# Performance work log

Hardware: AMD Instinct MI355X
Metric: run time of the kernel (lower is better)

## Reference

```python
import math
import jax, jax.numpy as jnp
import numpy as np

HEADS = 8
DIM_HEAD = 64
NUM_MEM_KV = 16


def alibi_slopes(heads):
    def pow2_slopes(n):
        start = 2 ** (-(2 ** -(math.log2(n) - 3)))
        return [start * (start ** i) for i in range(n)]
    if math.log2(heads).is_integer():
        return np.asarray(pow2_slopes(heads), dtype=np.float32)
    cp2 = 2 ** math.floor(math.log2(heads))
    extra = pow2_slopes(2 * cp2)[0::2][: heads - cp2]
    return np.asarray(pow2_slopes(cp2) + extra, dtype=np.float32)


def setup_inputs() -> dict:
    key = jax.random.key(0)
    ks = jax.random.split(key, 12)
    b, n, dim = 2, 2048, 512
    h, dh, mem = HEADS, DIM_HEAD, NUM_MEM_KV
    s = 0.02  # weight init scale for numerical sanity
    return {
        "x": jax.random.normal(ks[0], (b, n, dim), jnp.float32),
        "Wq": jax.random.normal(ks[1], (dim, h * dh), jnp.float32) * s,
        "Wk": jax.random.normal(ks[2], (dim, h * dh), jnp.float32) * s,
        "Wv": jax.random.normal(ks[3], (dim, h * dh), jnp.float32) * s,
        "mem_k": jax.random.normal(ks[4], (h, mem, dh), jnp.float32),
        "mem_v": jax.random.normal(ks[5], (h, mem, dh), jnp.float32),
        "pre_proj": jax.random.normal(ks[6], (h, h), jnp.float32),
        "post_proj": jax.random.normal(ks[7], (h, h), jnp.float32),
        "head_scale_params": jnp.ones((1, h, 1, 1), jnp.float32),
        "Wout": jax.random.normal(ks[8], (h * dh, dim), jnp.float32) * s,
        "bout": jnp.zeros((dim,), jnp.float32),
    }


def reference(x, Wq, Wk, Wv, mem_k, mem_v, pre_proj, post_proj,
              head_scale_params, Wout, bout):
    b, n, dim = x.shape
    h, dh, mem = HEADS, DIM_HEAD, NUM_MEM_KV
    scale = dh ** -0.5

    def split_heads(t):  # [b,n,h*dh] -> [b,h,n,dh]
        return t.reshape(b, n, h, dh).transpose(0, 2, 1, 3)

    q = split_heads(x @ Wq)
    k = split_heads(x @ Wk)
    v = split_heads(x @ Wv)

    # prepend learned memory key/values: k,v -> [b,h,mem+n,dh]
    k = jnp.concatenate([jnp.broadcast_to(mem_k, (b, h, mem, dh)), k], axis=2)
    v = jnp.concatenate([jnp.broadcast_to(mem_v, (b, h, mem, dh)), v], axis=2)
    j = mem + n

    dots = jnp.einsum('bhid,bhjd->bhij', q, k) * scale
    # talking heads (pre-softmax)
    dots = jnp.einsum('bhij,hk->bkij', dots, pre_proj)
    # alibi relative positional bias: arange(j) * slope per head
    slopes = jnp.asarray(alibi_slopes(h))  # [h]
    dots = dots + jnp.arange(j, dtype=dots.dtype)[None, None, None, :] * slopes[None, :, None, None]
    # causal mask (mem columns always visible); mask where col-mem > row
    neg = -jnp.finfo(dots.dtype).max
    causal = (jnp.arange(j)[None, :] - mem) > jnp.arange(n)[:, None]  # [n,j]
    dots = jnp.where(causal[None, None], neg, dots)

    attn = jax.nn.softmax(dots, axis=-1)
    # talking heads (post-softmax)
    attn = jnp.einsum('bhij,hk->bkij', attn, post_proj)

    out = jnp.einsum('bhij,bhjd->bhid', attn, v)
    out = out * head_scale_params
    out = out.transpose(0, 2, 1, 3).reshape(b, n, h * dh)
    return out @ Wout + bout
```

## Files before the change

kernel.cpp:

```cpp
#include <hip/hip_runtime.h>
#include <math.h>

namespace {
constexpr int B = 2;
constexpr int N = 2048;
constexpr int DIM = 512;
constexpr int H = 8;
constexpr int MEM = 16;
constexpr int J = MEM + N;
constexpr int CHUNK = 512;
constexpr int CMAXS = 5;
constexpr float S2 = 0.125f * 1.4426950408889634f;
constexpr size_t EPB = 17170432;
}

typedef __attribute__((ext_vector_type(8))) short short8;
typedef __attribute__((ext_vector_type(2))) float floatx2;
typedef __attribute__((ext_vector_type(4))) float floatx4;
typedef __attribute__((ext_vector_type(4))) unsigned short ushortx4;
typedef __attribute__((ext_vector_type(8))) unsigned short ushortx8;
typedef __attribute__((ext_vector_type(4))) unsigned int uintx4;

__device__ inline unsigned short f2bf(float f) {
    unsigned int u = __float_as_uint(f);
    u += 0x7fffu + ((u >> 16) & 1u);
    return (unsigned short)(u >> 16);
}
__device__ inline unsigned int pk2bf(float a, float b) {
    return ((__float_as_uint(a) + 0x8000u) >> 16) |
           ((__float_as_uint(b) + 0x8000u) & 0xffff0000u);
}

__global__ __launch_bounds__(256)
void x_conv(const float* __restrict__ x, unsigned short* __restrict__ x16)
{
    const size_t base = ((size_t)blockIdx.x * 256 + threadIdx.x) * 8;
    const float4 a = *(const float4*)(x + base);
    const float4 b = *(const float4*)(x + base + 4);
    ushortx8 o = { f2bf(a.x), f2bf(a.y), f2bf(a.z), f2bf(a.w),
                   f2bf(b.x), f2bf(b.y), f2bf(b.z), f2bf(b.w) };
    *(ushortx8*)(x16 + base) = o;
}

__global__ __launch_bounds__(256)
void wt_conv(const float* __restrict__ Wq, const float* __restrict__ Wk,
             const float* __restrict__ Wv, const float* __restrict__ Wo,
             unsigned short* __restrict__ tq, unsigned short* __restrict__ tk,
             unsigned short* __restrict__ tv, unsigned short* __restrict__ to_)
{
    const int z = blockIdx.z;
    const float* __restrict__ W = (z == 0) ? Wq : (z == 1) ? Wk : (z == 2) ? Wv : Wo;
    unsigned short* __restrict__ WT = (z == 0) ? tq : (z == 1) ? tk : (z == 2) ? tv : to_;
    const int k0 = blockIdx.x * 64, n0 = blockIdx.y * 64;

    __shared__ __align__(16) unsigned short tile[64][72];
    const int t = threadIdx.x;
    const int rrow = t >> 4, rcol = (t & 15) * 4;
#pragma unroll
    for (int rr = 0; rr < 4; ++rr) {
        const int row = rrow + rr * 16;
        const float4 v = *(const float4*)(W + (size_t)(k0 + row) * DIM + n0 + rcol);
        tile[rcol + 0][row] = f2bf(v.x);
        tile[rcol + 1][row] = f2bf(v.y);
        tile[rcol + 2][row] = f2bf(v.z);
        tile[rcol + 3][row] = f2bf(v.w);
    }
    __syncthreads();
    const int orow = t >> 2, oseg = (t & 3) * 16;
    *(ushortx8*)(WT + (size_t)(n0 + orow) * DIM + k0 + oseg) =
        *(const ushortx8*)(&tile[orow][oseg]);
    *(ushortx8*)(WT + (size_t)(n0 + orow) * DIM + k0 + oseg + 8) =
        *(const ushortx8*)(&tile[orow][oseg + 8]);
}

__global__ __launch_bounds__(256)
void qkv_gemm(const unsigned short* __restrict__ x16, const unsigned short* __restrict__ tq,
              const unsigned short* __restrict__ tk, const unsigned short* __restrict__ tv,
              unsigned short* __restrict__ q16, unsigned short* __restrict__ kcat,
              unsigned short* __restrict__ vt16)
{
    const int which = blockIdx.z;
    const unsigned short* __restrict__ WT = (which == 0) ? tq : (which == 1) ? tk : tv;
    const int t = threadIdx.x;
    const int lane = t & 63, w = t >> 6;
    const int iL = lane & 15, quad = lane >> 4;
    const int mb = blockIdx.x * 64;
    const int n0 = blockIdx.y * 64;

    __shared__ __align__(16) unsigned short As[2][64][32];
    __shared__ __align__(16) unsigned short Bs[2][64][32];

    const int r0 = t >> 2, s8 = (t & 3) * 8;

    floatx4 acc[4];
#pragma unroll
    for (int ng = 0; ng < 4; ++ng) acc[ng] = (floatx4){0.f, 0.f, 0.f, 0.f};

    {
        *(ushortx8*)(&As[0][r0][s8]) =
            *(const ushortx8*)(x16 + (size_t)(mb + r0) * DIM + s8);
        *(ushortx8*)(&Bs[0][r0][s8]) =
            *(const ushortx8*)(WT + (size_t)(n0 + r0) * DIM + s8);
    }
    __syncthreads();

#pragma unroll
    for (int it = 0; it < 16; ++it) {
        const int buf = it & 1;
        if (it + 1 < 16) {
            const int k0 = (it + 1) * 32;
            const ushortx8 av = *(const ushortx8*)(x16 + (size_t)(mb + r0) * DIM + k0 + s8);
            const ushortx8 bv = *(const ushortx8*)(WT + (size_t)(n0 + r0) * DIM + k0 + s8);
            *(ushortx8*)(&As[buf ^ 1][r0][s8]) = av;
            *(ushortx8*)(&Bs[buf ^ 1][r0][s8]) = bv;
        }
        const short8 af = *(const short8*)(&As[buf][w * 16 + iL][quad * 8]);
#pragma unroll
        for (int ng = 0; ng < 4; ++ng) {
            const short8 bf = *(const short8*)(&Bs[buf][ng * 16 + iL][quad * 8]);
            acc[ng] = __builtin_amdgcn_mfma_f32_16x16x32_bf16(af, bf, acc[ng], 0, 0, 0);
        }
        __syncthreads();
    }

    const int mbw = mb + w * 16;
    const int h0 = n0 >> 6;
    if (which == 2) {
#pragma unroll
        for (int ng = 0; ng < 4; ++ng) {
            const int d = ng * 16 + iL;
#pragma unroll
            for (int r = 0; r < 4; ++r) {
                const int m = mbw + quad * 4 + r;
                const int bb = m >> 11, ii = m & (N - 1);
                vt16[((size_t)(bb * H + h0) * 64 + d) * J + MEM + ii] = f2bf(acc[ng][r]);
            }
        }
    } else if (which == 1) {
#pragma unroll
        for (int ng = 0; ng < 4; ++ng) {
            const int d = ng * 16 + iL;
#pragma unroll
            for (int r = 0; r < 4; ++r) {
                const int m = mbw + quad * 4 + r;
                const int bb = m >> 11, ii = m & (N - 1);
                kcat[((size_t)bb * J + MEM + ii) * 512 + h0 * 64 + d] = f2bf(acc[ng][r]);
            }
        }
    } else {
#pragma unroll
        for (int ng = 0; ng < 4; ++ng) {
            const int d = ng * 16 + iL;
#pragma unroll
            for (int r = 0; r < 4; ++r) {
                const int m = mbw + quad * 4 + r;
                const int bb = m >> 11, ii = m & (N - 1);
                q16[((size_t)(bb * H + h0) * N + ii) * 64 + d] = f2bf(acc[ng][r]);
            }
        }
    }
}

__global__ void memkv_copy(const float* __restrict__ mem_k, const float* __restrict__ mem_v,
                           unsigned short* __restrict__ kcat, unsigned short* __restrict__ vt16)
{
    const int idx = blockIdx.x * 256 + threadIdx.x;
    if (idx >= H * MEM * 64) return;
    const int h0 = idx >> 10;
    const int rd = idx & 1023;
    const int r = rd >> 6, d = rd & 63;
    const unsigned short kk = f2bf(mem_k[idx]);
    const unsigned short vv = f2bf(mem_v[idx]);
#pragma unroll
    for (int bb = 0; bb < B; ++bb) {
        kcat[((size_t)bb * J + r) * 512 + h0 * 64 + d] = kk;
        vt16[((size_t)(bb * H + h0) * 64 + d) * J + r] = vv;
    }
}

__global__ __launch_bounds__(512, 4)
void attn_scores(const unsigned short* __restrict__ qb, const unsigned short* __restrict__ kc,
                 const float* __restrict__ prep, float* __restrict__ lbuf,
                 unsigned short* __restrict__ e16)
{
    const int tt = blockIdx.x, c = 4 - blockIdx.y, b = blockIdx.z;
    const int i0 = tt * 16;
    const int jlim = i0 + 32;
    const int jstart = c * CHUNK;
    if (jstart >= jlim) return;
    const int jend = min(jstart + CHUNK, jlim);
    const int nwin = (jend - jstart) >> 4;

    __shared__ __align__(16) unsigned short k_s[2][16][520];

    const int t = threadIdx.x;
    const int lane = t & 63, w = t >> 6;
    const int iL = lane & 15, quad = lane >> 4;
    const int i = i0 + iL;

    const size_t krowbase = (size_t)b * J * 512;

    auto STAGE = [&](int buf, int jw0) {
#pragma unroll
        for (int rr = 0; rr < 2; ++rr) {
            const int row = rr * 8 + w;
            const int j = jw0 + row;
            const char* src = (const char*)(kc + krowbase + (size_t)j * 512);
            __builtin_amdgcn_global_load_lds(
                (const __attribute__((address_space(1))) unsigned int*)(src + lane * 16),
                (__attribute__((address_space(3))) unsigned int*)(&k_s[buf][row][0]),
                16, 0, 0);
        }
    };

    STAGE(0, jstart);

    float pr[8];
#pragma unroll
    for (int h0 = 0; h0 < 8; ++h0) pr[h0] = prep[h0 * 8 + w];
    short8 qf[16];
#pragma unroll
    for (int ks = 0; ks < 16; ++ks) {
        const ushortx8 raw = *(const ushortx8*)(
            qb + ((size_t)(b * H + (ks >> 1)) * N + i0 + iL) * 64 + (ks & 1) * 32 + quad * 8);
        const float s = pr[ks >> 1];
        uintx4 u;
#pragma unroll
        for (int e2 = 0; e2 < 4; ++e2) {
            const float f0 = __uint_as_float((unsigned int)raw[e2 * 2] << 16) * s;
            const float f1 = __uint_as_float((unsigned int)raw[e2 * 2 + 1] << 16) * s;
            u[e2] = pk2bf(f0, f1);
        }
        qf[ks] = __builtin_bit_cast(short8, u);
    }
    __syncthreads();

    const float sl = 1.4426950408889634f / (float)(2 << w);
    const size_t ebase = (size_t)b * EPB + (size_t)(8 * tt * tt + 24 * tt) * 128;
    float l_acc = 0.f;

    for (int n = 0; n < nwin; ++n) {
        const int buf = n & 1;
        if (n + 1 < nwin) STAGE(buf ^ 1, jstart + (n + 1) * 16);
        const int jw0 = jstart + n * 16;

        floatx4 aE = {0.f, 0.f, 0.f, 0.f}, aO = {0.f, 0.f, 0.f, 0.f};
#pragma unroll
        for (int ks = 0; ks < 16; ks += 2) {
            const short8 f0 = *(const short8*)(&k_s[buf][iL][ks * 32 + quad * 8]);
            const short8 f1 = *(const short8*)(&k_s[buf][iL][(ks + 1) * 32 + quad * 8]);
            aE = __builtin_amdgcn_mfma_f32_16x16x32_bf16(f0, qf[ks], aE, 0, 0, 0);
            aO = __builtin_amdgcn_mfma_f32_16x16x32_bf16(f1, qf[ks + 1], aO, 0, 0, 0);
        }
        const floatx4 a = aE + aO;

#pragma unroll
        for (int r = 0; r < 4; ++r) {
            const int j = jw0 + quad * 4 + r;
            const int jm = j - MEM;
            const float e = (jm <= i)
                ? exp2f(fmaf(a[r], S2, sl * (float)(jm - i))) : 0.f;
            l_acc += e;
            e16[ebase + ((size_t)j * 16 + iL) * 8 + w] = f2bf(e);
        }
        __syncthreads();
    }

    l_acc += __shfl_xor(l_acc, 16);
    l_acc += __shfl_xor(l_acc, 32);
    if (quad == 0)
        atomicAdd(lbuf + ((size_t)(b * 128 + tt) * 8 + w) * 16 + iL, l_acc);
}

__global__ __launch_bounds__(256)
void attn_pv2(const unsigned short* __restrict__ e16, const unsigned short* __restrict__ vt,
              const float* __restrict__ postp, const float* __restrict__ hsp,
              const float* __restrict__ lbuf, float* __restrict__ ao)
{
    const int tt = blockIdx.x, c = 4 - blockIdx.y, b = blockIdx.z;
    const int i0 = tt * 16;
    const int jlim = i0 + 32;
    const int jstart = c * CHUNK;
    if (jstart >= jlim) return;
    const int jend = min(jstart + CHUNK, jlim);
    const int nw = (jend - jstart + 31) >> 5;

    __shared__ __align__(16) unsigned short p2s[2][8][16][40];
    __shared__ __align__(16) float post_s[64];

    const int t = threadIdx.x;
    if (t < 64) post_s[t] = postp[t] * hsp[t & 7];

    const int lane = t & 63, w = t >> 6;
    const int iL = lane & 15, quad = lane >> 4;
    const int dW = w * 16 + iL;
    const int i_p = t & 15;
    const int jj = t >> 4;
    const size_t ebase = (size_t)b * EPB + (size_t)(8 * tt * tt + 24 * tt) * 128;
    const unsigned short* __restrict__ ep = e16 + ebase + (size_t)i_p * 8;

    float linv[8];
#pragma unroll
    for (int h1 = 0; h1 < 8; ++h1)
        linv[h1] = 1.0f / lbuf[((size_t)(b * 128 + tt) * 8 + h1) * 16 + i_p];

    floatx4 y[8];
#pragma unroll
    for (int h2 = 0; h2 < 8; ++h2) y[h2] = (floatx4){0.f, 0.f, 0.f, 0.f};

    ushortx8 evA[2], evB[2], evC[2];
    {
        const int j0c = jstart + jj * 2;
        int ja = min(j0c, jend - 1), jb2 = min(j0c + 1, jend - 1);
        evA[0] = *(const ushortx8*)(ep + (size_t)(ja * 16) * 8);
        evA[1] = *(const ushortx8*)(ep + (size_t)(jb2 * 16) * 8);
        ja = min(j0c + 32, jend - 1); jb2 = min(j0c + 33, jend - 1);
        evB[0] = *(const ushortx8*)(ep + (size_t)(ja * 16) * 8);
        evB[1] = *(const ushortx8*)(ep + (size_t)(jb2 * 16) * 8);
        ja = min(j0c + 64, jend - 1); jb2 = min(j0c + 65, jend - 1);
        evC[0] = *(const ushortx8*)(ep + (size_t)(ja * 16) * 8);
        evC[1] = *(const ushortx8*)(ep + (size_t)(jb2 * 16) * 8);
    }
    __syncthreads();

    for (int n = 0; n < nw; ++n) {
        const int jw0 = jstart + n * 32;
        const int buf = n & 1;

        int jbv = jw0 + quad * 8;
        if (jbv > J - 8) jbv = J - 8;
        short8 bF[8];
#pragma unroll
        for (int h2 = 0; h2 < 8; ++h2)
            bF[h2] = *(const short8*)(vt + ((size_t)(b * H + h2) * 64 + dW) * J + jbv);

        ushortx8 evT0, evT1;
        {
            const int wn = (n + 3 < nw) ? n + 3 : nw - 1;
            const int j0n = jstart + wn * 32 + jj * 2;
            const int ja = min(j0n, jend - 1), jb2 = min(j0n + 1, jend - 1);
            evT0 = *(const ushortx8*)(ep + (size_t)(ja * 16) * 8);
            evT1 = *(const ushortx8*)(ep + (size_t)(jb2 * 16) * 8);
        }

        floatx2 p2v[2][4];
#pragma unroll
        for (int s = 0; s < 2; ++s) {
#pragma unroll
            for (int q = 0; q < 4; ++q) p2v[s][q] = (floatx2){0.f, 0.f};
            const int j = jw0 + jj * 2 + s;
            if (j < jend) {
#pragma unroll
                for (int h1 = 0; h1 < 8; ++h1) {
                    const float e = __uint_as_float(
                        (unsigned int)(unsigned short)evA[s][h1] << 16) * linv[h1];
                    const floatx2* po = (const floatx2*)(&post_s[h1 * 8]);
                    p2v[s][0] += e * po[0];
                    p2v[s][1] += e * po[1];
                    p2v[s][2] += e * po[2];
                    p2v[s][3] += e * po[3];
                }
            }
        }
#pragma unroll
        for (int h2 = 0; h2 < 8; ++h2)
            *(unsigned int*)(&p2s[buf][h2][i_p][jj * 2]) =
                pk2bf(p2v[0][h2 >> 1][h2 & 1], p2v[1][h2 >> 1][h2 & 1]);
        __syncthreads();

#pragma unroll
        for (int h2 = 0; h2 < 8; ++h2) {
            const short8 aF = *(const short8*)(&p2s[buf][h2][iL][quad * 8]);
            y[h2] = __builtin_amdgcn_mfma_f32_16x16x32_bf16(aF, bF[h2], y[h2], 0, 0, 0);
        }
        evA[0] = evB[0]; evA[1] = evB[1];
        evB[0] = evC[0]; evB[1] = evC[1];
        evC[0] = evT0;   evC[1] = evT1;
    }

#pragma unroll
    for (int h2 = 0; h2 < 8; ++h2) {
#pragma unroll
        for (int r = 0; r < 4; ++r) {
            const int ii = i0 + quad * 4 + r;
            atomicAdd(ao + ((size_t)b * N + ii) * DIM + h2 * 64 + dW, y[h2][r]);
        }
    }
}

__global__ __launch_bounds__(256)
void out_gemm(const float* __restrict__ ain, const unsigned short* __restrict__ WT,
              const float* __restrict__ bo, float* __restrict__ out)
{
    const int t = threadIdx.x;
    const int lane = t & 63, w = t >> 6;
    const int iL = lane & 15, quad = lane >> 4;
    const int mb = blockIdx.x * 64;
    const int n0 = blockIdx.y * 64;

    __shared__ __align__(16) unsigned short As[2][64][32];
    __shared__ __align__(16) unsigned short Bs[2][64][32];

    const int ar0 = t >> 3, as4 = (t & 7) * 4;
    const int br0 = t >> 2, bs8 = (t & 3) * 8;

    floatx4 acc[4];
#pragma unroll
    for (int ng = 0; ng < 4; ++ng) acc[ng] = (floatx4){0.f, 0.f, 0.f, 0.f};

    {
        const float4 v0 = *(const float4*)(ain + (size_t)(mb + ar0) * DIM + as4);
        const float4 v1 = *(const float4*)(ain + (size_t)(mb + ar0 + 32) * DIM + as4);
        ushortx4 o0 = { f2bf(v0.x), f2bf(v0.y), f2bf(v0.z), f2bf(v0.w) };
        ushortx4 o1 = { f2bf(v1.x), f2bf(v1.y), f2bf(v1.z), f2bf(v1.w) };
        *(ushortx4*)(&As[0][ar0][as4]) = o0;
        *(ushortx4*)(&As[0][ar0 + 32][as4]) = o1;
        *(ushortx8*)(&Bs[0][br0][bs8]) =
            *(const ushortx8*)(WT + (size_t)(n0 + br0) * DIM + bs8);
    }
    __syncthreads();

#pragma unroll
    for (int it = 0; it < 16; ++it) {
        const int buf = it & 1;
        if (it + 1 < 16) {
            const int k0 = (it + 1) * 32;
            const float4 v0 = *(const float4*)(ain + (size_t)(mb + ar0) * DIM + k0 + as4);
            const float4 v1 = *(const float4*)(ain + (size_t)(mb + ar0 + 32) * DIM + k0 + as4);
            const ushortx8 bv =
                *(const ushortx8*)(WT + (size_t)(n0 + br0) * DIM + k0 + bs8);
            ushortx4 o0 = { f2bf(v0.x), f2bf(v0.y), f2bf(v0.z), f2bf(v0.w) };
            ushortx4 o1 = { f2bf(v1.x), f2bf(v1.y), f2bf(v1.z), f2bf(v1.w) };
            *(ushortx4*)(&As[buf ^ 1][ar0][as4]) = o0;
            *(ushortx4*)(&As[buf ^ 1][ar0 + 32][as4]) = o1;
            *(ushortx8*)(&Bs[buf ^ 1][br0][bs8]) = bv;
        }
        const short8 af = *(const short8*)(&As[buf][w * 16 + iL][quad * 8]);
#pragma unroll
        for (int ng = 0; ng < 4; ++ng) {
            const short8 bf = *(const short8*)(&Bs[buf][ng * 16 + iL][quad * 8]);
            acc[ng] = __builtin_amdgcn_mfma_f32_16x16x32_bf16(af, bf, acc[ng], 0, 0, 0);
        }
        __syncthreads();
    }

    const int mbw = mb + w * 16;
#pragma unroll
    for (int ng = 0; ng < 4; ++ng) {
        const int n = n0 + ng * 16 + iL;
        const float bias = bo[n];
#pragma unroll
        for (int r = 0; r < 4; ++r) {
            const int m = mbw + quad * 4 + r;
            out[(size_t)m * DIM + n] = acc[ng][r] + bias;
        }
    }
}

extern "C" void kernel_launch(void* const* d_in, const int* in_sizes, int n_in,
                              void* d_out, int out_size, void* d_ws, size_t ws_size,
                              hipStream_t stream)
{
    (void)in_sizes; (void)n_in; (void)out_size; (void)ws_size;
    const float* x      = (const float*)d_in[0];
    const float* Wq     = (const float*)d_in[1];
    const float* Wk     = (const float*)d_in[2];
    const float* Wv     = (const float*)d_in[3];
    const float* mem_k  = (const float*)d_in[4];
    const float* mem_v  = (const float*)d_in[5];
    const float* pre_p  = (const float*)d_in[6];
    const float* post_p = (const float*)d_in[7];
    const float* hs     = (const float*)d_in[8];
    const float* Wo     = (const float*)d_in[9];
    const float* bo     = (const float*)d_in[10];
    float* out = (float*)d_out;

    constexpr size_t NAO  = (size_t)B * N * DIM;
    constexpr size_t NLB  = (size_t)B * 128 * H * 16;
    constexpr size_t NW   = (size_t)DIM * DIM;
    constexpr size_t NQ   = (size_t)B * H * N * 64;
    constexpr size_t NK   = (size_t)B * J * 512;
    constexpr size_t NX   = (size_t)B * N * DIM;

    float* ws = (float*)d_ws;
    float* ao   = ws;
    float* lbuf = ao + NAO;
    unsigned short* wtq  = (unsigned short*)(lbuf + NLB);
    unsigned short* wtk  = wtq + NW;
    unsigned short* wtv  = wtk + NW;
    unsigned short* wto  = wtv + NW;
    unsigned short* q16  = wto + NW;
    unsigned short* kcat = q16 + NQ;
    unsigned short* v16  = kcat + NK;
    unsigned short* x16  = v16 + NK;
    unsigned short* e16  = x16 + NX;

    x_conv<<<dim3(1024), 256, 0, stream>>>(x, x16);
    wt_conv<<<dim3(8, 8, 4), 256, 0, stream>>>(Wq, Wk, Wv, Wo, wtq, wtk, wtv, wto);
    qkv_gemm<<<dim3(64, 8, 3), 256, 0, stream>>>(x16, wtq, wtk, wtv, q16, kcat, v16);
    memkv_copy<<<dim3(32), 256, 0, stream>>>(mem_k, mem_v, kcat, v16);
    hipMemsetAsync(ao, 0, (NAO + NLB) * sizeof(float), stream);
    attn_scores<<<dim3(128, CMAXS, B), 512, 0, stream>>>(q16, kcat, pre_p, lbuf, e16);
    attn_pv2<<<dim3(128, CMAXS, B), 256, 0, stream>>>(e16, v16, post_p, hs, lbuf, ao);
    out_gemm<<<dim3(64, 8), 256, 0, stream>>>(ao, wto, bo, out);
}
```

Baseline: 266.6 us.

## Restructure attn_scores: per-head raw QK MFMAs, apply pre_proj mixing after, drop LDS staging

```diff
diff --git a/kernel.cpp b/kernel.cpp
--- a/kernel.cpp
+++ b/kernel.cpp
@@ -7,7 +7,7 @@
 constexpr int DIM = 512;
 constexpr int H = 8;
 constexpr int MEM = 16;
-constexpr int J = MEM + N;
+constexpr int J = MEM + 16 * 128;
 constexpr int CHUNK = 512;
 constexpr int CMAXS = 5;
 constexpr float S2 = 0.125f * 1.4426950408889634f;
@@ -178,7 +178,7 @@
     }
 }
 
-__global__ __launch_bounds__(512, 4)
+__global__ __launch_bounds__(256, 3)
 void attn_scores(const unsigned short* __restrict__ qb, const unsigned short* __restrict__ kc,
                  const float* __restrict__ prep, float* __restrict__ lbuf,
                  unsigned short* __restrict__ e16)
@@ -189,87 +189,95 @@
     const int jstart = c * CHUNK;
     if (jstart >= jlim) return;
     const int jend = min(jstart + CHUNK, jlim);
-    const int nwin = (jend - jstart) >> 4;
-
-    __shared__ __align__(16) unsigned short k_s[2][16][520];
-
+
+    __shared__ float pre_s[64];
     const int t = threadIdx.x;
+    if (t < 64) pre_s[t] = prep[t];
+
     const int lane = t & 63, w = t >> 6;
     const int iL = lane & 15, quad = lane >> 4;
     const int i = i0 + iL;
 
-    const size_t krowbase = (size_t)b * J * 512;
-
-    auto STAGE = [&](int buf, int jw0) {
-#pragma unroll
-        for (int rr = 0; rr < 2; ++rr) {
-            const int row = rr * 8 + w;
-            const int j = jw0 + row;
-            const char* src = (const char*)(kc + krowbase + (size_t)j * 512);
-            __builtin_amdgcn_global_load_lds(
-                (const __attribute__((address_space(1))) unsigned int*)(src + lane * 16),
-                (__attribute__((address_space(3))) unsigned int*)(&k_s[buf][row][0]),
-                16, 0, 0);
-        }
-    };
-
-    STAGE(0, jstart);
-
-    float pr[8];
-#pragma unroll
-    for (int h0 = 0; h0 < 8; ++h0) pr[h0] = prep[h0 * 8 + w];
     short8 qf[16];
 #pragma unroll
     for (int ks = 0; ks < 16; ++ks) {
         const ushortx8 raw = *(const ushortx8*)(
             qb + ((size_t)(b * H + (ks >> 1)) * N + i0 + iL) * 64 + (ks & 1) * 32 + quad * 8);
-        const float s = pr[ks >> 1];
-        uintx4 u;
-#pragma unroll
-        for (int e2 = 0; e2 < 4; ++e2) {
-            const float f0 = __uint_as_float((unsigned int)raw[e2 * 2] << 16) * s;
-            const float f1 = __uint_as_float((unsigned int)raw[e2 * 2 + 1] << 16) * s;
-            u[e2] = pk2bf(f0, f1);
-        }
-        qf[ks] = __builtin_bit_cast(short8, u);
-    }
+        qf[ks] = __builtin_bit_cast(short8, raw);
+    }
+#pragma unroll
+    for (int ks = 0; ks < 16; ++ks)
+        asm volatile("" : "+v"(qf[ks]));
+
     __syncthreads();
 
-    const float sl = 1.4426950408889634f / (float)(2 << w);
     const size_t ebase = (size_t)b * EPB + (size_t)(8 * tt * tt + 24 * tt) * 128;
-    float l_acc = 0.f;
-
-    for (int n = 0; n < nwin; ++n) {
-        const int buf = n & 1;
-        if (n + 1 < nwin) STAGE(buf ^ 1, jstart + (n + 1) * 16);
-        const int jw0 = jstart + n * 16;
-
-        floatx4 aE = {0.f, 0.f, 0.f, 0.f}, aO = {0.f, 0.f, 0.f, 0.f};
-#pragma unroll
-        for (int ks = 0; ks < 16; ks += 2) {
-            const short8 f0 = *(const short8*)(&k_s[buf][iL][ks * 32 + quad * 8]);
-            const short8 f1 = *(const short8*)(&k_s[buf][iL][(ks + 1) * 32 + quad * 8]);
-            aE = __builtin_amdgcn_mfma_f32_16x16x32_bf16(f0, qf[ks], aE, 0, 0, 0);
-            aO = __builtin_amdgcn_mfma_f32_16x16x32_bf16(f1, qf[ks + 1], aO, 0, 0, 0);
-        }
-        const floatx4 a = aE + aO;
-
+    float l_acc[8];
+#pragma unroll
+    for (int h1 = 0; h1 < 8; ++h1) l_acc[h1] = 0.f;
+
+    for (int j0 = jstart + w * 16; j0 < jend; j0 += 64) {
+        const unsigned short* kr = kc + ((size_t)b * J + j0 + iL) * 512 + quad * 8;
+
+        short8 c0 = *(const short8*)(kr);
+        short8 c1 = *(const short8*)(kr + 32);
+        short8 n0 = *(const short8*)(kr + 64);
+        short8 n1 = *(const short8*)(kr + 96);
+
+        floatx4 a[8];
+#pragma unroll
+        for (int h0 = 0; h0 < 8; ++h0) {
+            short8 p0, p1;
+            if (h0 < 6) {
+                p0 = *(const short8*)(kr + (h0 + 2) * 64);
+                p1 = *(const short8*)(kr + (h0 + 2) * 64 + 32);
+            }
+            floatx4 acc = {0.f, 0.f, 0.f, 0.f};
+            acc = __builtin_amdgcn_mfma_f32_16x16x32_bf16(c0, qf[2 * h0], acc, 0, 0, 0);
+            acc = __builtin_amdgcn_mfma_f32_16x16x32_bf16(c1, qf[2 * h0 + 1], acc, 0, 0, 0);
+            a[h0] = acc;
+            c0 = n0; c1 = n1; n0 = p0; n1 = p1;
+        }
+
+        unsigned int epk[4][4];
+        float etmp[4];
+#pragma unroll
+        for (int h1 = 0; h1 < 8; ++h1) {
+            const float slopeE = 1.4426950408889634f / (float)(2 << h1);
+            floatx2 d01 = {0.f, 0.f}, d23 = {0.f, 0.f};
+#pragma unroll
+            for (int h0 = 0; h0 < 8; ++h0) {
+                const float p = pre_s[h0 * 8 + h1];
+                d01 += (floatx2){a[h0][0], a[h0][1]} * p;
+                d23 += (floatx2){a[h0][2], a[h0][3]} * p;
+            }
+            const float dd[4] = {d01[0], d01[1], d23[0], d23[1]};
+#pragma unroll
+            for (int r = 0; r < 4; ++r) {
+                const int j = j0 + quad * 4 + r;
+                const int jm = j - MEM;
+                const float e = (jm <= i)
+                    ? exp2f(fmaf(dd[r], S2, slopeE * (float)(jm - i))) : 0.f;
+                l_acc[h1] += e;
+                if (h1 & 1) epk[r][h1 >> 1] = pk2bf(etmp[r], e);
+                else        etmp[r] = e;
+            }
+        }
 #pragma unroll
         for (int r = 0; r < 4; ++r) {
-            const int j = jw0 + quad * 4 + r;
-            const int jm = j - MEM;
-            const float e = (jm <= i)
-                ? exp2f(fmaf(a[r], S2, sl * (float)(jm - i))) : 0.f;
-            l_acc += e;
-            e16[ebase + ((size_t)j * 16 + iL) * 8 + w] = f2bf(e);
-        }
-        __syncthreads();
-    }
-
-    l_acc += __shfl_xor(l_acc, 16);
-    l_acc += __shfl_xor(l_acc, 32);
-    if (quad == 0)
-        atomicAdd(lbuf + ((size_t)(b * 128 + tt) * 8 + w) * 16 + iL, l_acc);
+            uint4 o = make_uint4(epk[r][0], epk[r][1], epk[r][2], epk[r][3]);
+            *(uint4*)(e16 + ebase + (size_t)((j0 + quad * 4 + r) * 16 + iL) * 8) = o;
+        }
+    }
+
+#pragma unroll
+    for (int h1 = 0; h1 < 8; ++h1) {
+        float v = l_acc[h1];
+        v += __shfl_xor(v, 16);
+        v += __shfl_xor(v, 32);
+        if (quad == 0)
+            atomicAdd(lbuf + ((size_t)(b * 128 + tt) * 8 + h1) * 16 + iL, v);
+    }
 }
 
 __global__ __launch_bounds__(256)
@@ -500,7 +508,7 @@
     qkv_gemm<<<dim3(64, 8, 3), 256, 0, stream>>>(x16, wtq, wtk, wtv, q16, kcat, v16);
     memkv_copy<<<dim3(32), 256, 0, stream>>>(mem_k, mem_v, kcat, v16);
     hipMemsetAsync(ao, 0, (NAO + NLB) * sizeof(float), stream);
-    attn_scores<<<dim3(128, CMAXS, B), 512, 0, stream>>>(q16, kcat, pre_p, lbuf, e16);
+    attn_scores<<<dim3(128, CMAXS, B), 256, 0, stream>>>(q16, kcat, pre_p, lbuf, e16);
     attn_pv2<<<dim3(128, CMAXS, B), 256, 0, stream>>>(e16, v16, post_p, hs, lbuf, ao);
     out_gemm<<<dim3(64, 8), 256, 0, stream>>>(ao, wto, bo, out);
 }
```

Result: slower. 369.1 us (+38.5%).
